# Kernel tuning notes

Hardware: AMD Instinct MI355X
Metric: run time of the kernel (lower is better)

## Reference

```python
import jax, jax.numpy as jnp
import numpy as np

N = 100000       # num nodes
E = 1600000      # num edges
IN_DIM = 128
HID = 128
HEADS = 4
HEAD_DIM = HID // HEADS  # 32
NEG_SLOPE = 0.2
LN_EPS = 1e-5


def _glorot(key, shape):
    fan_in, fan_out = shape[-1], shape[0]
    limit = float(np.sqrt(6.0 / (fan_in + fan_out)))
    return jax.random.uniform(key, shape, jnp.float32, -limit, limit)


def setup_inputs() -> dict:
    key = jax.random.key(0)
    ks = jax.random.split(key, 16)
    return {
        "x": jax.random.normal(ks[0], (N, IN_DIM), jnp.float32),
        "edge_index": jax.random.randint(ks[1], (2, E), 0, N, jnp.int64),
        # embedding Linear(IN_DIM -> HID)
        "W_emb": _glorot(ks[2], (HID, IN_DIM)),
        "b_emb": jnp.zeros((HID,), jnp.float32),
        # E8 layer weight (F.linear, no bias)
        "W_e8": _glorot(ks[3], (HID, HID)),
        # GATConv: lin weight [HID, HEADS*HEAD_DIM], attention vectors, output bias
        "W_gat": _glorot(ks[4], (HEADS * HEAD_DIM, HID)),
        "att_src": _glorot(ks[5], (HEADS, HEAD_DIM)),
        "att_dst": _glorot(ks[6], (HEADS, HEAD_DIM)),
        "b_gat": jnp.zeros((HEADS * HEAD_DIM,), jnp.float32),
        # fusion Linear(2*HID -> HID)
        "W_fus": _glorot(ks[7], (HID, 2 * HID)),
        "b_fus": jnp.zeros((HID,), jnp.float32),
        # LayerNorm(HID)
        "gamma": jnp.ones((HID,), jnp.float32),
        "beta": jnp.zeros((HID,), jnp.float32),
        # readout MLP HID -> HID//2 -> 1
        "W_r1": _glorot(ks[8], (HID // 2, HID)),
        "b_r1": jnp.zeros((HID // 2,), jnp.float32),
        "W_r2": _glorot(ks[9], (1, HID // 2)),
        "b_r2": jnp.zeros((1,), jnp.float32),
    }


def reference(x, edge_index, W_emb, b_emb, W_e8, W_gat, att_src, att_dst,
              b_gat, W_fus, b_fus, gamma, beta, W_r1, b_r1, W_r2, b_r2):
    row = edge_index[0]  # src
    col = edge_index[1]  # dst

    # embedding
    h = x @ W_emb.T + b_emb          # [N, HID]
    res = h

    # --- E8: sparse normalized-adjacency matmul + linear ---
    deg = jax.ops.segment_sum(jnp.ones((E,), h.dtype), col, num_segments=N)
    dinv = jnp.where(deg > 0, deg ** -0.5, 0.0)
    vals = dinv[row] * dinv[col]                       # [E]
    agg = jax.ops.segment_sum(h[col] * vals[:, None], row, num_segments=N)
    x_e8 = agg @ W_e8.T                                # [N, HID]

    # --- GATConv (heads=4, concat, add_self_loops) ---
    loop = jnp.arange(N, dtype=row.dtype)
    src = jnp.concatenate([row, loop])                 # [E+N]
    dst = jnp.concatenate([col, loop])
    g = (h @ W_gat.T).reshape(N, HEADS, HEAD_DIM)      # [N, H, C]
    a_src = (g * att_src).sum(-1)                      # [N, H]
    a_dst = (g * att_dst).sum(-1)
    e = jax.nn.leaky_relu(a_src[src] + a_dst[dst], NEG_SLOPE)  # [E+N, H]
    m = jax.ops.segment_max(e, dst, num_segments=N)    # scatter-softmax max
    e = jnp.exp(e - m[dst])
    s = jax.ops.segment_sum(e, dst, num_segments=N)
    alpha = e / (s[dst] + 1e-16)                       # [E+N, H]
    msg = g[src] * alpha[..., None]                    # [E+N, H, C]
    x_gat = jax.ops.segment_sum(msg, dst, num_segments=N).reshape(N, HEADS * HEAD_DIM) + b_gat

    # --- fusion + residual + LayerNorm + ReLU ---
    f = jnp.concatenate([x_e8, x_gat], axis=-1) @ W_fus.T + b_fus
    z = f + res
    mu = z.mean(-1, keepdims=True)
    var = ((z - mu) ** 2).mean(-1, keepdims=True)
    z = (z - mu) * jax.lax.rsqrt(var + LN_EPS) * gamma + beta
    z = jax.nn.relu(z)  # dropout is identity in eval mode

    # --- readout MLP + sigmoid ---
    r = jax.nn.relu(z @ W_r1.T + b_r1)
    out = jax.nn.sigmoid(r @ W_r2.T + b_r2)            # [N, 1]
    return out
```

## Files before the change

### kernel.cpp

```cpp
#include <hip/hip_runtime.h>
#include <hip/hip_bf16.h>
#include <math.h>

#define NWIN 8
#define NCHUNK 256
#define CAP 64

typedef __attribute__((ext_vector_type(8))) short bf16x8;
typedef __attribute__((ext_vector_type(4))) float f32x4;

__device__ __forceinline__ float us2f(unsigned short u) {
    return __uint_as_float(((unsigned)u) << 16);
}
__device__ __forceinline__ unsigned short f2bf(float f) {
    unsigned u = __float_as_uint(f);
    u += 0x7FFF + ((u >> 16) & 1);
    return (unsigned short)(u >> 16);
}

__global__ void prep_kernel(const float* __restrict__ b_gat,
                            const float* __restrict__ W_fus, const float* __restrict__ b_fus,
                            float* __restrict__ bfus2) {
    int t = threadIdx.x;
    float acc = b_fus[t];
    for (int k = 0; k < 128; k++)
        acc += b_gat[k] * W_fus[t * 256 + 128 + k];
    bfus2[t] = acc;
}

__global__ void convert_w(const float* __restrict__ We, const float* __restrict__ W8,
                          const float* __restrict__ Wg, const float* __restrict__ Wf,
                          unsigned short* __restrict__ W16) {
    int i = blockIdx.x * 256 + threadIdx.x;
    if (i >= 81920) return;
    float v;
    if (i < 16384) v = We[i];
    else if (i < 32768) v = W8[i - 16384];
    else if (i < 49152) v = Wg[i - 32768];
    else v = Wf[i - 49152];
    W16[i] = f2bf(v);
}

__global__ __launch_bounds__(256) void fill_win(
    const int* __restrict__ row, const int* __restrict__ col,
    int* __restrict__ cnt, int* __restrict__ adjF, int E, int N, int win) {
    int b = blockIdx.x;
    int w = b & (NWIN - 1);
    int chunk = b >> 3;
    int lo = w * win, hi = lo + win;
    int per = (E + NCHUNK - 1) / NCHUNK;
    per = (per + 1) & ~1;
    int s = chunk * per;
    int e_end = s + per; if (e_end > E) e_end = E;
    for (int i = s + threadIdx.x * 2; i < e_end; i += 512) {
        int2 rv, cv;
        if (i + 1 < e_end) {
            rv = *(const int2*)(row + i);
            cv = *(const int2*)(col + i);
        } else {
            rv.x = row[i]; rv.y = -1;
            cv.x = col[i]; cv.y = 0;
        }
        if (cv.x >= lo && cv.x < hi) {
            int p = atomicAdd(&cnt[cv.x], 1);
            if (p < CAP) adjF[(size_t)cv.x * CAP + p] = rv.x;
        }
        int k2 = N + rv.x;
        if (k2 >= lo && k2 < hi) {
            int p = atomicAdd(&cnt[k2], 1);
            if (p < CAP) adjF[(size_t)k2 * CAP + p] = cv.x;
        }
        if (rv.y >= 0) {
            if (cv.y >= lo && cv.y < hi) {
                int p = atomicAdd(&cnt[cv.y], 1);
                if (p < CAP) adjF[(size_t)cv.y * CAP + p] = rv.y;
            }
            int k3 = N + rv.y;
            if (k3 >= lo && k3 < hi) {
                int p = atomicAdd(&cnt[k3], 1);
                if (p < CAP) adjF[(size_t)k3 * CAP + p] = cv.y;
            }
        }
    }
}

__global__ void dinv_kernel(const int* __restrict__ cnt, float* __restrict__ dinv, int N) {
    int i = blockIdx.x * 256 + threadIdx.x;
    if (i < N) {
        int d = cnt[i];
        dinv[i] = d > 0 ? rsqrtf((float)d) : 0.0f;
    }
}

template <bool A_FP32, bool HAS_BIAS, bool OUT_F32, bool OUT_BF16, bool OUT_SC, bool OUT_ATT>
__global__ __launch_bounds__(256) void gemm_mfma(
    const void* __restrict__ A_, const unsigned short* __restrict__ W16,
    const float* __restrict__ bias, float* __restrict__ Cf,
    unsigned short* __restrict__ C16, const float* __restrict__ rsc,
    unsigned short* __restrict__ Csc, const float* __restrict__ attS,
    const float* __restrict__ attD, float* __restrict__ aS, float* __restrict__ aD,
    int n) {
    const int t = threadIdx.x;
    const int wave = t >> 6, lane = t & 63;
    const int quad = lane >> 4, ln = lane & 15;
    const int row0 = blockIdx.x * 128 + wave * 32;
    const int kq = quad * 8;

    f32x4 zero = {0.f, 0.f, 0.f, 0.f};
    f32x4 acc[2][8];
#pragma unroll
    for (int i = 0; i < 2; i++)
#pragma unroll
        for (int j = 0; j < 8; j++) acc[i][j] = zero;

#pragma unroll
    for (int ks = 0; ks < 4; ks++) {
        bf16x8 a[2];
#pragma unroll
        for (int mt = 0; mt < 2; mt++) {
            int row = row0 + mt * 16 + ln;
            if (row >= n) row = n - 1;
            if (A_FP32) {
                const float* ap = (const float*)A_ + (size_t)row * 128 + ks * 32 + kq;
                float4 f0 = *(const float4*)ap;
                float4 f1 = *(const float4*)(ap + 4);
                bf16x8 v;
                v[0] = (short)f2bf(f0.x); v[1] = (short)f2bf(f0.y);
                v[2] = (short)f2bf(f0.z); v[3] = (short)f2bf(f0.w);
                v[4] = (short)f2bf(f1.x); v[5] = (short)f2bf(f1.y);
                v[6] = (short)f2bf(f1.z); v[7] = (short)f2bf(f1.w);
                a[mt] = v;
            } else {
                a[mt] = *(const bf16x8*)((const unsigned short*)A_ +
                                         (size_t)row * 128 + ks * 32 + kq);
            }
        }
#pragma unroll
        for (int nt = 0; nt < 8; nt++) {
            bf16x8 b = *(const bf16x8*)(W16 + (size_t)(nt * 16 + ln) * 128 + ks * 32 + kq);
            acc[0][nt] = __builtin_amdgcn_mfma_f32_16x16x32_bf16(a[0], b, acc[0][nt], 0, 0, 0);
            acc[1][nt] = __builtin_amdgcn_mfma_f32_16x16x32_bf16(a[1], b, acc[1][nt], 0, 0, 0);
        }
    }

    float bv[8];
    if (HAS_BIAS) {
#pragma unroll
        for (int nt = 0; nt < 8; nt++) bv[nt] = bias[nt * 16 + ln];
    }
    float asv[8], adv[8];
    if (OUT_ATT) {
#pragma unroll
        for (int nt = 0; nt < 8; nt++) {
            int idx = (nt >> 1) * 32 + (nt & 1) * 16 + ln;
            asv[nt] = attS[idx];
            adv[nt] = attD[idx];
        }
    }
#pragma unroll
    for (int mt = 0; mt < 2; mt++) {
        int rbase = row0 + mt * 16 + quad * 4;
#pragma unroll
        for (int reg = 0; reg < 4; reg++) {
            int row = rbase + reg;
            if (row >= n) continue;
            float sc = OUT_SC ? rsc[row] : 0.f;
            if (OUT_ATT) {
                float ps[4] = {0.f, 0.f, 0.f, 0.f};
                float pd[4] = {0.f, 0.f, 0.f, 0.f};
#pragma unroll
                for (int nt = 0; nt < 8; nt++) {
                    float v = acc[mt][nt][reg];
                    ps[nt >> 1] += v * asv[nt];
                    pd[nt >> 1] += v * adv[nt];
                }
#pragma unroll
                for (int m = 1; m < 16; m <<= 1) {
#pragma unroll
                    for (int hh = 0; hh < 4; hh++) {
                        ps[hh] += __shfl_xor(ps[hh], m);
                        pd[hh] += __shfl_xor(pd[hh], m);
                    }
                }
                if (ln == 0) {
                    *(float4*)&aS[(size_t)row * 4] = make_float4(ps[0], ps[1], ps[2], ps[3]);
                    *(float4*)&aD[(size_t)row * 4] = make_float4(pd[0], pd[1], pd[2], pd[3]);
                }
            }
#pragma unroll
            for (int nt = 0; nt < 8; nt++) {
                float v = acc[mt][nt][reg];
                if (HAS_BIAS) v += bv[nt];
                int col = nt * 16 + ln;
                if (OUT_F32) Cf[(size_t)row * 128 + col] = v;
                if (OUT_BF16) C16[(size_t)row * 128 + col] = f2bf(v);
                if (OUT_SC) Csc[(size_t)row * 128 + col] = f2bf(v * sc);
            }
        }
    }
}

__global__ __launch_bounds__(256) void fusion_ln_mfma(
    const unsigned short* __restrict__ xe816, const unsigned short* __restrict__ xg16,
    const unsigned short* __restrict__ Wf16,
    const float* __restrict__ bfus2, const float* __restrict__ h,
    const float* __restrict__ gamma, const float* __restrict__ beta,
    float* __restrict__ z, int n) {
    const int t = threadIdx.x;
    const int wave = t >> 6, lane = t & 63;
    const int quad = lane >> 4, ln = lane & 15;
    const int row0 = blockIdx.x * 128 + wave * 32;
    const int kq = quad * 8;

    f32x4 zero = {0.f, 0.f, 0.f, 0.f};
    f32x4 acc[2][8];
#pragma unroll
    for (int i = 0; i < 2; i++)
#pragma unroll
        for (int j = 0; j < 8; j++) acc[i][j] = zero;

    for (int half = 0; half < 2; half++) {
        const unsigned short* A = half ? xg16 : xe816;
#pragma unroll
        for (int ks = 0; ks < 4; ks++) {
            bf16x8 a[2];
#pragma unroll
            for (int mt = 0; mt < 2; mt++) {
                int row = row0 + mt * 16 + ln;
                if (row >= n) row = n - 1;
                a[mt] = *(const bf16x8*)(A + (size_t)row * 128 + ks * 32 + kq);
            }
#pragma unroll
            for (int nt = 0; nt < 8; nt++) {
                bf16x8 b = *(const bf16x8*)(Wf16 + (size_t)(nt * 16 + ln) * 256 +
                                            half * 128 + ks * 32 + kq);
                acc[0][nt] = __builtin_amdgcn_mfma_f32_16x16x32_bf16(a[0], b, acc[0][nt], 0, 0, 0);
                acc[1][nt] = __builtin_amdgcn_mfma_f32_16x16x32_bf16(a[1], b, acc[1][nt], 0, 0, 0);
            }
        }
    }

    float bv[8], gm[8], bt[8];
#pragma unroll
    for (int nt = 0; nt < 8; nt++) {
        int c = nt * 16 + ln;
        bv[nt] = bfus2[c]; gm[nt] = gamma[c]; bt[nt] = beta[c];
    }
#pragma unroll
    for (int mt = 0; mt < 2; mt++) {
#pragma unroll
        for (int reg = 0; reg < 4; reg++) {
            int row = row0 + mt * 16 + quad * 4 + reg;
            if (row >= n) continue;
            float v[8];
            float s1 = 0.f, s2 = 0.f;
#pragma unroll
            for (int nt = 0; nt < 8; nt++) {
                float x = acc[mt][nt][reg] + bv[nt] + h[(size_t)row * 128 + nt * 16 + ln];
                v[nt] = x; s1 += x; s2 += x * x;
            }
#pragma unroll
            for (int m = 1; m < 16; m <<= 1) {
                s1 += __shfl_xor(s1, m);
                s2 += __shfl_xor(s2, m);
            }
            float mu = s1 * (1.f / 128.f);
            float var = s2 * (1.f / 128.f) - mu * mu;
            float inv = rsqrtf(var + 1e-5f);
#pragma unroll
            for (int nt = 0; nt < 8; nt++) {
                float o = (v[nt] - mu) * inv * gm[nt] + bt[nt];
                o = o > 0.f ? o : 0.f;
                z[(size_t)row * 128 + nt * 16 + ln] = o;
            }
        }
    }
}

__global__ __launch_bounds__(256) void e8_gather(
    const int* __restrict__ cnt, const int* __restrict__ adjF,
    const float* __restrict__ dinv, const unsigned short* __restrict__ hd16,
    unsigned short* __restrict__ agg16, int N) {
    int r = blockIdx.x * 4 + (threadIdx.x >> 6);
    int lane = threadIdx.x & 63;
    if (r >= N) return;
    int key = N + r;
    int m = min(cnt[key], CAP);
    int av = (lane < m) ? adjF[(size_t)key * CAP + lane] : 0;
    float ax = 0.f, ay = 0.f;
    int j = 0;
    for (; j + 4 <= m; j += 4) {
        int c0 = __shfl(av, j), c1 = __shfl(av, j + 1);
        int c2 = __shfl(av, j + 2), c3 = __shfl(av, j + 3);
        ushort2 h0 = *(const ushort2*)&hd16[(size_t)c0 * 128 + lane * 2];
        ushort2 h1 = *(const ushort2*)&hd16[(size_t)c1 * 128 + lane * 2];
        ushort2 h2 = *(const ushort2*)&hd16[(size_t)c2 * 128 + lane * 2];
        ushort2 h3 = *(const ushort2*)&hd16[(size_t)c3 * 128 + lane * 2];
        ax += us2f(h0.x) + us2f(h1.x) + us2f(h2.x) + us2f(h3.x);
        ay += us2f(h0.y) + us2f(h1.y) + us2f(h2.y) + us2f(h3.y);
    }
    for (; j < m; j++) {
        int c = __shfl(av, j);
        ushort2 hv = *(const ushort2*)&hd16[(size_t)c * 128 + lane * 2];
        ax += us2f(hv.x);
        ay += us2f(hv.y);
    }
    float dr = dinv[r];
    ushort2 o; o.x = f2bf(ax * dr); o.y = f2bf(ay * dr);
    *(ushort2*)&agg16[(size_t)r * 128 + lane * 2] = o;
}

__global__ __launch_bounds__(256) void gat_gather(
    const int* __restrict__ cnt, const int* __restrict__ adjF,
    const float* __restrict__ a_src, const float* __restrict__ a_dst,
    const unsigned short* __restrict__ g16, unsigned short* __restrict__ xg16, int N) {
    int d = blockIdx.x * 4 + (threadIdx.x >> 6);
    int lane = threadIdx.x & 63;
    if (d >= N) return;
    int hd = lane >> 4;
    float ad = a_dst[d * 4 + hd];

    float e = a_src[d * 4 + hd] + ad; e = e > 0.f ? e : 0.2f * e;
    float m0 = e, l = 1.f;
    ushort2 gv0 = *(const ushort2*)&g16[(size_t)d * 128 + lane * 2];
    float accx = us2f(gv0.x), accy = us2f(gv0.y);

    int mm = min(cnt[d], CAP);
    int av = (lane < mm) ? adjF[(size_t)d * CAP + lane] : 0;
    int j = 0;
    for (; j + 2 <= mm; j += 2) {
        int s0 = __shfl(av, j), s1 = __shfl(av, j + 1);
        float t0 = a_src[s0 * 4 + hd] + ad; t0 = t0 > 0.f ? t0 : 0.2f * t0;
        float t1 = a_src[s1 * 4 + hd] + ad; t1 = t1 > 0.f ? t1 : 0.2f * t1;
        ushort2 gu0 = *(const ushort2*)&g16[(size_t)s0 * 128 + lane * 2];
        ushort2 gu1 = *(const ushort2*)&g16[(size_t)s1 * 128 + lane * 2];
        float mn = fmaxf(m0, fmaxf(t0, t1));
        float sc = __expf(m0 - mn), w0 = __expf(t0 - mn), w1 = __expf(t1 - mn);
        accx = accx * sc + w0 * us2f(gu0.x) + w1 * us2f(gu1.x);
        accy = accy * sc + w0 * us2f(gu0.y) + w1 * us2f(gu1.y);
        l = l * sc + w0 + w1;
        m0 = mn;
    }
    for (; j < mm; j++) {
        int s = __shfl(av, j);
        float t0 = a_src[s * 4 + hd] + ad; t0 = t0 > 0.f ? t0 : 0.2f * t0;
        ushort2 gu = *(const ushort2*)&g16[(size_t)s * 128 + lane * 2];
        float mn = fmaxf(m0, t0);
        float sc = __expf(m0 - mn), w = __expf(t0 - mn);
        accx = accx * sc + w * us2f(gu.x);
        accy = accy * sc + w * us2f(gu.y);
        l = l * sc + w;
        m0 = mn;
    }
    float inv = 1.f / l;
    ushort2 o; o.x = f2bf(accx * inv); o.y = f2bf(accy * inv);
    *(ushort2*)&xg16[(size_t)d * 128 + lane * 2] = o;
}

__global__ __launch_bounds__(256) void readout_kernel(
    const float* __restrict__ z, const float* __restrict__ W1, const float* __restrict__ b1,
    const float* __restrict__ W2, const float* __restrict__ b2,
    float* __restrict__ out, int N) {
    __shared__ float zs[32 * 132];
    __shared__ float wlds[64 * 132];
    __shared__ float w2s[64];
    __shared__ float b1s[64];
    const int t = threadIdx.x;
    const int row0 = blockIdx.x * 32;

    for (int i = 0; i < 4; i++) {
        int idx = i * 256 + t;
        int r = idx >> 5, c4 = idx & 31;
        float4 v = make_float4(0.f, 0.f, 0.f, 0.f);
        if (row0 + r < N) v = *(const float4*)&z[(size_t)(row0 + r) * 128 + c4 * 4];
        *(float4*)&zs[r * 132 + c4 * 4] = v;
    }
    for (int i = 0; i < 8; i++) {
        int idx = i * 256 + t;
        int o = idx >> 5, c4 = idx & 31;
        *(float4*)&wlds[o * 132 + c4 * 4] = *(const float4*)&W1[o * 128 + c4 * 4];
    }
    if (t < 64) { w2s[t] = W2[t]; b1s[t] = b1[t]; }
    __syncthreads();

    const int rg = t >> 4;
    const int cg = t & 15;
    float acc[2][4] = {};
    const float* z0 = &zs[(rg * 2) * 132];
    const float* z1 = z0 + 132;
    for (int k4 = 0; k4 < 32; k4++) {
        float4 a0 = *(const float4*)&z0[k4 * 4];
        float4 a1 = *(const float4*)&z1[k4 * 4];
#pragma unroll
        for (int j = 0; j < 4; j++) {
            float4 wv = *(const float4*)&wlds[(cg * 4 + j) * 132 + k4 * 4];
            acc[0][j] += a0.x * wv.x + a0.y * wv.y + a0.z * wv.z + a0.w * wv.w;
            acc[1][j] += a1.x * wv.x + a1.y * wv.y + a1.z * wv.z + a1.w * wv.w;
        }
    }
    float p0 = 0.f, p1 = 0.f;
#pragma unroll
    for (int j = 0; j < 4; j++) {
        int o = cg * 4 + j;
        float r0 = acc[0][j] + b1s[o]; r0 = r0 > 0.f ? r0 : 0.f;
        float r1 = acc[1][j] + b1s[o]; r1 = r1 > 0.f ? r1 : 0.f;
        p0 += r0 * w2s[o]; p1 += r1 * w2s[o];
    }
    for (int off = 8; off > 0; off >>= 1) {
        p0 += __shfl_down(p0, off, 16);
        p1 += __shfl_down(p1, off, 16);
    }
    if (cg == 0) {
        float bb = b2[0];
        int r0i = row0 + rg * 2, r1i = r0i + 1;
        if (r0i < N) out[r0i] = 1.f / (1.f + __expf(-(p0 + bb)));
        if (r1i < N) out[r1i] = 1.f / (1.f + __expf(-(p1 + bb)));
    }
}

extern "C" void kernel_launch(void* const* d_in, const int* in_sizes, int n_in,
                              void* d_out, int out_size, void* d_ws, size_t ws_size,
                              hipStream_t stream) {
    const float* x     = (const float*)d_in[0];
    const int*   ei    = (const int*)d_in[1];
    const float* W_emb = (const float*)d_in[2];
    const float* b_emb = (const float*)d_in[3];
    const float* W_e8  = (const float*)d_in[4];
    const float* W_gat = (const float*)d_in[5];
    const float* att_s = (const float*)d_in[6];
    const float* att_d = (const float*)d_in[7];
    const float* b_gat = (const float*)d_in[8];
    const float* W_fus = (const float*)d_in[9];
    const float* b_fus = (const float*)d_in[10];
    const float* gamma = (const float*)d_in[11];
    const float* beta  = (const float*)d_in[12];
    const float* W_r1  = (const float*)d_in[13];
    const float* b_r1  = (const float*)d_in[14];
    const float* W_r2  = (const float*)d_in[15];
    const float* b_r2  = (const float*)d_in[16];

    const int N = in_sizes[0] / 128;
    const int E = in_sizes[1] / 2;
    const int* rowp = ei;
    const int* colp = ei + E;
    const int total = 2 * N;
    const int win = (total + NWIN - 1) / NWIN;
    const int GB = (N + 127) / 128;

    const size_t NF = (size_t)N * 128;
    char* base = (char*)d_ws;
    float* B_h             = (float*)base;
    unsigned short* hd16   = (unsigned short*)(base + NF * 4);
    unsigned short* bufA   = hd16 + NF;
    unsigned short* xe816  = bufA + NF;
    unsigned short* g16    = xe816 + NF;
    float* B_z             = (float*)(g16 + NF);
    int*   adjF            = (int*)B_z;
    float* dinv  = B_z + NF;
    float* a_src = dinv + N;
    float* a_dst = a_src + (size_t)4 * N;
    float* bfus2 = a_dst + (size_t)4 * N;
    unsigned short* W16a = (unsigned short*)(bfus2 + 128);
    unsigned short* We16 = W16a;
    unsigned short* W816 = W16a + 16384;
    unsigned short* Wg16 = W16a + 32768;
    unsigned short* Wf16 = W16a + 49152;
    int* cnt = (int*)(W16a + 81920);

    prep_kernel<<<1, 128, 0, stream>>>(b_gat, W_fus, b_fus, bfus2);
    convert_w<<<320, 256, 0, stream>>>(W_emb, W_e8, W_gat, W_fus, W16a);
    hipMemsetAsync(cnt, 0, (size_t)total * 4, stream);
    fill_win<<<NWIN * NCHUNK, 256, 0, stream>>>(rowp, colp, cnt, adjF, E, N, win);
    dinv_kernel<<<(N + 255) / 256, 256, 0, stream>>>(cnt, dinv, N);

    gemm_mfma<true, true, true, false, true, false><<<GB, 256, 0, stream>>>(
        x, We16, b_emb, B_h, nullptr, dinv, hd16, nullptr, nullptr, nullptr, nullptr, N);

    e8_gather<<<(N + 3) / 4, 256, 0, stream>>>(cnt, adjF, dinv, hd16, bufA, N);
    gemm_mfma<false, false, false, true, false, false><<<GB, 256, 0, stream>>>(
        bufA, W816, nullptr, nullptr, xe816, nullptr, nullptr,
        nullptr, nullptr, nullptr, nullptr, N);

    gemm_mfma<true, false, false, true, false, true><<<GB, 256, 0, stream>>>(
        B_h, Wg16, nullptr, nullptr, g16, nullptr, nullptr,
        att_s, att_d, a_src, a_dst, N);
    gat_gather<<<(N + 3) / 4, 256, 0, stream>>>(cnt, adjF, a_src, a_dst, g16, bufA, N);

    fusion_ln_mfma<<<GB, 256, 0, stream>>>(xe816, bufA, Wf16, bfus2, B_h,
                                           gamma, beta, B_z, N);

    readout_kernel<<<(N + 31) / 32, 256, 0, stream>>>(B_z, W_r1, b_r1, W_r2, b_r2,
                                                      (float*)d_out, N);
}
```

Baseline: 628.0 us.

## Store h and z in bf16, merge setup kernels, widen gather and fill loops

Stores the embedding output h and the LayerNorm output z as bf16 instead of fp32, which cuts memory traffic in the GAT GEMM, the fusion residual and the readout. The three setup launches (bias prep, weight conversion, count memset) are merged into one kernel. fill_win now reads edges as 4-wide nontemporal vectors and writes adjacency with nontemporal stores. The gather loops are unrolled to 8 and 4 neighbors to raise memory-level parallelism. The extra bf16 rounding of h and z adds some numerical error.

```diff
diff --git a/kernel.cpp b/kernel.cpp
--- a/kernel.cpp
+++ b/kernel.cpp
@@ -8,6 +8,7 @@
 
 typedef __attribute__((ext_vector_type(8))) short bf16x8;
 typedef __attribute__((ext_vector_type(4))) float f32x4;
+typedef __attribute__((ext_vector_type(4))) int i32x4;
 
 __device__ __forceinline__ float us2f(unsigned short u) {
     return __uint_as_float(((unsigned)u) << 16);
@@ -18,27 +19,36 @@
     return (unsigned short)(u >> 16);
 }
 
-__global__ void prep_kernel(const float* __restrict__ b_gat,
-                            const float* __restrict__ W_fus, const float* __restrict__ b_fus,
-                            float* __restrict__ bfus2) {
-    int t = threadIdx.x;
-    float acc = b_fus[t];
-    for (int k = 0; k < 128; k++)
-        acc += b_gat[k] * W_fus[t * 256 + 128 + k];
-    bfus2[t] = acc;
-}
-
-__global__ void convert_w(const float* __restrict__ We, const float* __restrict__ W8,
-                          const float* __restrict__ Wg, const float* __restrict__ Wf,
-                          unsigned short* __restrict__ W16) {
-    int i = blockIdx.x * 256 + threadIdx.x;
-    if (i >= 81920) return;
-    float v;
-    if (i < 16384) v = We[i];
-    else if (i < 32768) v = W8[i - 16384];
-    else if (i < 49152) v = Wg[i - 32768];
-    else v = Wf[i - 49152];
-    W16[i] = f2bf(v);
+__global__ void setup_kernel(const float* __restrict__ b_gat, const float* __restrict__ W_fus,
+                             const float* __restrict__ b_fus, float* __restrict__ bfus2,
+                             const float* __restrict__ We, const float* __restrict__ W8,
+                             const float* __restrict__ Wg, unsigned short* __restrict__ W16,
+                             int* __restrict__ cnt, int total) {
+    int b = blockIdx.x;
+    if (b == 0) {
+        int t = threadIdx.x;
+        if (t < 128) {
+            float acc = b_fus[t];
+            for (int k = 0; k < 128; k++)
+                acc += b_gat[k] * W_fus[t * 256 + 128 + k];
+            bfus2[t] = acc;
+        }
+        return;
+    }
+    if (b <= 320) {
+        int i = (b - 1) * 256 + threadIdx.x;
+        if (i < 81920) {
+            float v;
+            if (i < 16384) v = We[i];
+            else if (i < 32768) v = W8[i - 16384];
+            else if (i < 49152) v = Wg[i - 32768];
+            else v = W_fus[i - 49152];
+            W16[i] = f2bf(v);
+        }
+        return;
+    }
+    int i = (b - 321) * 256 + threadIdx.x;
+    if (i < total) cnt[i] = 0;
 }
 
 __global__ __launch_bounds__(256) void fill_win(
@@ -49,37 +59,38 @@
     int chunk = b >> 3;
     int lo = w * win, hi = lo + win;
     int per = (E + NCHUNK - 1) / NCHUNK;
-    per = (per + 1) & ~1;
+    per = (per + 3) & ~3;
     int s = chunk * per;
     int e_end = s + per; if (e_end > E) e_end = E;
-    for (int i = s + threadIdx.x * 2; i < e_end; i += 512) {
-        int2 rv, cv;
-        if (i + 1 < e_end) {
-            rv = *(const int2*)(row + i);
-            cv = *(const int2*)(col + i);
-        } else {
-            rv.x = row[i]; rv.y = -1;
-            cv.x = col[i]; cv.y = 0;
-        }
-        if (cv.x >= lo && cv.x < hi) {
-            int p = atomicAdd(&cnt[cv.x], 1);
-            if (p < CAP) adjF[(size_t)cv.x * CAP + p] = rv.x;
-        }
-        int k2 = N + rv.x;
+
+    int i = s + threadIdx.x * 4;
+    for (; i + 4 <= e_end; i += 1024) {
+        i32x4 rv = __builtin_nontemporal_load((const i32x4*)(row + i));
+        i32x4 cv = __builtin_nontemporal_load((const i32x4*)(col + i));
+#pragma unroll
+        for (int q = 0; q < 4; q++) {
+            int r = rv[q], c = cv[q];
+            if (c >= lo && c < hi) {
+                int p = atomicAdd(&cnt[c], 1);
+                if (p < CAP) __builtin_nontemporal_store(r, &adjF[(size_t)c * CAP + p]);
+            }
+            int k2 = N + r;
+            if (k2 >= lo && k2 < hi) {
+                int p = atomicAdd(&cnt[k2], 1);
+                if (p < CAP) __builtin_nontemporal_store(c, &adjF[(size_t)k2 * CAP + p]);
+            }
+        }
+    }
+    for (; i < e_end; i++) {
+        int r = row[i], c = col[i];
+        if (c >= lo && c < hi) {
+            int p = atomicAdd(&cnt[c], 1);
+            if (p < CAP) adjF[(size_t)c * CAP + p] = r;
+        }
+        int k2 = N + r;
         if (k2 >= lo && k2 < hi) {
             int p = atomicAdd(&cnt[k2], 1);
-            if (p < CAP) adjF[(size_t)k2 * CAP + p] = cv.x;
-        }
-        if (rv.y >= 0) {
-            if (cv.y >= lo && cv.y < hi) {
-                int p = atomicAdd(&cnt[cv.y], 1);
-                if (p < CAP) adjF[(size_t)cv.y * CAP + p] = rv.y;
-            }
-            int k3 = N + rv.y;
-            if (k3 >= lo && k3 < hi) {
-                int p = atomicAdd(&cnt[k3], 1);
-                if (p < CAP) adjF[(size_t)k3 * CAP + p] = cv.y;
-            }
+            if (p < CAP) adjF[(size_t)k2 * CAP + p] = c;
         }
     }
 }
@@ -92,14 +103,13 @@
     }
 }
 
-template <bool A_FP32, bool HAS_BIAS, bool OUT_F32, bool OUT_BF16, bool OUT_SC, bool OUT_ATT>
+template <bool A_FP32, bool HAS_BIAS, bool OUT_BF16, bool OUT_SC, bool OUT_ATT>
 __global__ __launch_bounds__(256) void gemm_mfma(
     const void* __restrict__ A_, const unsigned short* __restrict__ W16,
-    const float* __restrict__ bias, float* __restrict__ Cf,
-    unsigned short* __restrict__ C16, const float* __restrict__ rsc,
-    unsigned short* __restrict__ Csc, const float* __restrict__ attS,
-    const float* __restrict__ attD, float* __restrict__ aS, float* __restrict__ aD,
-    int n) {
+    const float* __restrict__ bias, unsigned short* __restrict__ C16,
+    const float* __restrict__ rsc, unsigned short* __restrict__ Csc,
+    const float* __restrict__ attS, const float* __restrict__ attD,
+    float* __restrict__ aS, float* __restrict__ aD, int n) {
     const int t = threadIdx.x;
     const int wave = t >> 6, lane = t & 63;
     const int quad = lane >> 4, ln = lane & 15;
@@ -192,7 +202,6 @@
                 float v = acc[mt][nt][reg];
                 if (HAS_BIAS) v += bv[nt];
                 int col = nt * 16 + ln;
-                if (OUT_F32) Cf[(size_t)row * 128 + col] = v;
                 if (OUT_BF16) C16[(size_t)row * 128 + col] = f2bf(v);
                 if (OUT_SC) Csc[(size_t)row * 128 + col] = f2bf(v * sc);
             }
@@ -203,9 +212,9 @@
 __global__ __launch_bounds__(256) void fusion_ln_mfma(
     const unsigned short* __restrict__ xe816, const unsigned short* __restrict__ xg16,
     const unsigned short* __restrict__ Wf16,
-    const float* __restrict__ bfus2, const float* __restrict__ h,
+    const float* __restrict__ bfus2, const unsigned short* __restrict__ h16,
     const float* __restrict__ gamma, const float* __restrict__ beta,
-    float* __restrict__ z, int n) {
+    unsigned short* __restrict__ z16, int n) {
     const int t = threadIdx.x;
     const int wave = t >> 6, lane = t & 63;
     const int quad = lane >> 4, ln = lane & 15;
@@ -256,7 +265,8 @@
             float s1 = 0.f, s2 = 0.f;
 #pragma unroll
             for (int nt = 0; nt < 8; nt++) {
-                float x = acc[mt][nt][reg] + bv[nt] + h[(size_t)row * 128 + nt * 16 + ln];
+                float x = acc[mt][nt][reg] + bv[nt] +
+                          us2f(h16[(size_t)row * 128 + nt * 16 + ln]);
                 v[nt] = x; s1 += x; s2 += x * x;
             }
 #pragma unroll
@@ -271,7 +281,7 @@
             for (int nt = 0; nt < 8; nt++) {
                 float o = (v[nt] - mu) * inv * gm[nt] + bt[nt];
                 o = o > 0.f ? o : 0.f;
-                z[(size_t)row * 128 + nt * 16 + ln] = o;
+                z16[(size_t)row * 128 + nt * 16 + ln] = f2bf(o);
             }
         }
     }
@@ -289,15 +299,15 @@
     int av = (lane < m) ? adjF[(size_t)key * CAP + lane] : 0;
     float ax = 0.f, ay = 0.f;
     int j = 0;
-    for (; j + 4 <= m; j += 4) {
-        int c0 = __shfl(av, j), c1 = __shfl(av, j + 1);
-        int c2 = __shfl(av, j + 2), c3 = __shfl(av, j + 3);
-        ushort2 h0 = *(const ushort2*)&hd16[(size_t)c0 * 128 + lane * 2];
-        ushort2 h1 = *(const ushort2*)&hd16[(size_t)c1 * 128 + lane * 2];
-        ushort2 h2 = *(const ushort2*)&hd16[(size_t)c2 * 128 + lane * 2];
-        ushort2 h3 = *(const ushort2*)&hd16[(size_t)c3 * 128 + lane * 2];
-        ax += us2f(h0.x) + us2f(h1.x) + us2f(h2.x) + us2f(h3.x);
-        ay += us2f(h0.y) + us2f(h1.y) + us2f(h2.y) + us2f(h3.y);
+    for (; j + 8 <= m; j += 8) {
+        int c[8]; ushort2 hv[8];
+#pragma unroll
+        for (int q = 0; q < 8; q++) c[q] = __shfl(av, j + q);
+#pragma unroll
+        for (int q = 0; q < 8; q++)
+            hv[q] = *(const ushort2*)&hd16[(size_t)c[q] * 128 + lane * 2];
+#pragma unroll
+        for (int q = 0; q < 8; q++) { ax += us2f(hv[q].x); ay += us2f(hv[q].y); }
     }
     for (; j < m; j++) {
         int c = __shfl(av, j);
@@ -328,17 +338,34 @@
     int mm = min(cnt[d], CAP);
     int av = (lane < mm) ? adjF[(size_t)d * CAP + lane] : 0;
     int j = 0;
-    for (; j + 2 <= mm; j += 2) {
-        int s0 = __shfl(av, j), s1 = __shfl(av, j + 1);
-        float t0 = a_src[s0 * 4 + hd] + ad; t0 = t0 > 0.f ? t0 : 0.2f * t0;
-        float t1 = a_src[s1 * 4 + hd] + ad; t1 = t1 > 0.f ? t1 : 0.2f * t1;
-        ushort2 gu0 = *(const ushort2*)&g16[(size_t)s0 * 128 + lane * 2];
-        ushort2 gu1 = *(const ushort2*)&g16[(size_t)s1 * 128 + lane * 2];
-        float mn = fmaxf(m0, fmaxf(t0, t1));
-        float sc = __expf(m0 - mn), w0 = __expf(t0 - mn), w1 = __expf(t1 - mn);
-        accx = accx * sc + w0 * us2f(gu0.x) + w1 * us2f(gu1.x);
-        accy = accy * sc + w0 * us2f(gu0.y) + w1 * us2f(gu1.y);
-        l = l * sc + w0 + w1;
+    for (; j + 4 <= mm; j += 4) {
+        int s[4]; float tv[4]; ushort2 gu[4];
+#pragma unroll
+        for (int q = 0; q < 4; q++) s[q] = __shfl(av, j + q);
+#pragma unroll
+        for (int q = 0; q < 4; q++) tv[q] = a_src[s[q] * 4 + hd];
+#pragma unroll
+        for (int q = 0; q < 4; q++)
+            gu[q] = *(const ushort2*)&g16[(size_t)s[q] * 128 + lane * 2];
+        float mn = m0;
+#pragma unroll
+        for (int q = 0; q < 4; q++) {
+            tv[q] += ad;
+            tv[q] = tv[q] > 0.f ? tv[q] : 0.2f * tv[q];
+            mn = fmaxf(mn, tv[q]);
+        }
+        float sc = __expf(m0 - mn);
+        float wsum = 0.f, axp = 0.f, ayp = 0.f;
+#pragma unroll
+        for (int q = 0; q < 4; q++) {
+            float wq = __expf(tv[q] - mn);
+            wsum += wq;
+            axp += wq * us2f(gu[q].x);
+            ayp += wq * us2f(gu[q].y);
+        }
+        accx = accx * sc + axp;
+        accy = accy * sc + ayp;
+        l = l * sc + wsum;
         m0 = mn;
     }
     for (; j < mm; j++) {
@@ -358,9 +385,9 @@
 }
 
 __global__ __launch_bounds__(256) void readout_kernel(
-    const float* __restrict__ z, const float* __restrict__ W1, const float* __restrict__ b1,
-    const float* __restrict__ W2, const float* __restrict__ b2,
-    float* __restrict__ out, int N) {
+    const unsigned short* __restrict__ z16, const float* __restrict__ W1,
+    const float* __restrict__ b1, const float* __restrict__ W2,
+    const float* __restrict__ b2, float* __restrict__ out, int N) {
     __shared__ float zs[32 * 132];
     __shared__ float wlds[64 * 132];
     __shared__ float w2s[64];
@@ -372,7 +399,10 @@
         int idx = i * 256 + t;
         int r = idx >> 5, c4 = idx & 31;
         float4 v = make_float4(0.f, 0.f, 0.f, 0.f);
-        if (row0 + r < N) v = *(const float4*)&z[(size_t)(row0 + r) * 128 + c4 * 4];
+        if (row0 + r < N) {
+            ushort4 u = *(const ushort4*)&z16[(size_t)(row0 + r) * 128 + c4 * 4];
+            v = make_float4(us2f(u.x), us2f(u.y), us2f(u.z), us2f(u.w));
+        }
         *(float4*)&zs[r * 132 + c4 * 4] = v;
     }
     for (int i = 0; i < 8; i++) {
@@ -449,14 +479,14 @@
 
     const size_t NF = (size_t)N * 128;
     char* base = (char*)d_ws;
-    float* B_h             = (float*)base;
-    unsigned short* hd16   = (unsigned short*)(base + NF * 4);
-    unsigned short* bufA   = hd16 + NF;
-    unsigned short* xe816  = bufA + NF;
-    unsigned short* g16    = xe816 + NF;
-    float* B_z             = (float*)(g16 + NF);
-    int*   adjF            = (int*)B_z;
-    float* dinv  = B_z + NF;
+    unsigned short* h16   = (unsigned short*)base;
+    unsigned short* hd16  = h16 + NF;
+    unsigned short* bufA  = hd16 + NF;
+    unsigned short* xe816 = bufA + NF;
+    unsigned short* g16   = xe816 + NF;
+    int*            adjF  = (int*)(g16 + NF);
+    unsigned short* z16   = (unsigned short*)adjF;
+    float* dinv  = (float*)(adjF + NF);
     float* a_src = dinv + N;
     float* a_dst = a_src + (size_t)4 * N;
     float* bfus2 = a_dst + (size_t)4 * N;
@@ -467,28 +497,27 @@
     unsigned short* Wf16 = W16a + 49152;
     int* cnt = (int*)(W16a + 81920);
 
-    prep_kernel<<<1, 128, 0, stream>>>(b_gat, W_fus, b_fus, bfus2);
-    convert_w<<<320, 256, 0, stream>>>(W_emb, W_e8, W_gat, W_fus, W16a);
-    hipMemsetAsync(cnt, 0, (size_t)total * 4, stream);
+    int setup_grid = 321 + (total + 255) / 256;
+    setup_kernel<<<setup_grid, 256, 0, stream>>>(b_gat, W_fus, b_fus, bfus2,
+                                                 W_emb, W_e8, W_gat, W16a, cnt, total);
     fill_win<<<NWIN * NCHUNK, 256, 0, stream>>>(rowp, colp, cnt, adjF, E, N, win);
     dinv_kernel<<<(N + 255) / 256, 256, 0, stream>>>(cnt, dinv, N);
 
-    gemm_mfma<true, true, true, false, true, false><<<GB, 256, 0, stream>>>(
-        x, We16, b_emb, B_h, nullptr, dinv, hd16, nullptr, nullptr, nullptr, nullptr, N);
+    gemm_mfma<true, true, true, true, false><<<GB, 256, 0, stream>>>(
+        x, We16, b_emb, h16, dinv, hd16, nullptr, nullptr, nullptr, nullptr, N);
 
     e8_gather<<<(N + 3) / 4, 256, 0, stream>>>(cnt, adjF, dinv, hd16, bufA, N);
-    gemm_mfma<false, false, false, true, false, false><<<GB, 256, 0, stream>>>(
-        bufA, W816, nullptr, nullptr, xe816, nullptr, nullptr,
-        nullptr, nullptr, nullptr, nullptr, N);
-
-    gemm_mfma<true, false, false, true, false, true><<<GB, 256, 0, stream>>>(
-        B_h, Wg16, nullptr, nullptr, g16, nullptr, nullptr,
-        att_s, att_d, a_src, a_dst, N);
+    gemm_mfma<false, false, true, false, false><<<GB, 256, 0, stream>>>(
+        bufA, W816, nullptr, xe816, nullptr, nullptr, nullptr, nullptr,
+        nullptr, nullptr, N);
+
+    gemm_mfma<false, false, true, false, true><<<GB, 256, 0, stream>>>(
+        h16, Wg16, nullptr, g16, nullptr, nullptr, att_s, att_d, a_src, a_dst, N);
     gat_gather<<<(N + 3) / 4, 256, 0, stream>>>(cnt, adjF, a_src, a_dst, g16, bufA, N);
 
-    fusion_ln_mfma<<<GB, 256, 0, stream>>>(xe816, bufA, Wf16, bfus2, B_h,
-                                           gamma, beta, B_z, N);
-
-    readout_kernel<<<(N + 31) / 32, 256, 0, stream>>>(B_z, W_r1, b_r1, W_r2, b_r2,
+    fusion_ln_mfma<<<GB, 256, 0, stream>>>(xe816, bufA, Wf16, bfus2, h16,
+                                           gamma, beta, z16, N);
+
+    readout_kernel<<<(N + 31) / 32, 256, 0, stream>>>(z16, W_r1, b_r1, W_r2, b_r2,
                                                       (float*)d_out, N);
 }
```

New measurement: 638.8 us. No clear change (+1.7%).
